# Optimization experiments

Measured on AMD Instinct MI355X. Metric: run time of the kernel, lower is better.

## Reference

```python
import jax, jax.numpy as jnp
import numpy as np
from jax.scipy.special import logsumexp

R, B, D, V, F = 64, 64, 256, 32000, 7
DFF = 4 * D
K_ACT, TOPK_N, TOP_M = 6, 4, 2
NEG = -1e30
C_TAU = 0.20333333  # mean of (1 - alpha) over taus alpha in {0.5, 0.9, 0.99}; zero prev state


def _hex_neighbors(side=8):
    offs = [(1, 0), (-1, 0), (0, 1), (0, -1), (1, -1), (-1, 1)]
    idx = [[((r + dr) % side) * side + (c + dc) % side for dr, dc in offs]
           for r in range(side) for c in range(side)]
    return jnp.array(idx, dtype=jnp.int32)


def setup_inputs() -> dict:
    key = jax.random.key(0)
    ks = jax.random.split(key, 12)
    def rn(k, shp, s):
        return jax.random.normal(k, shp, dtype=jnp.float32) * s
    return {
        "x_per_region": rn(ks[0], (R, B, D), 1.0),
        "targets": jax.random.randint(ks[1], (B,), 0, V),
        "neighbor_indices": _hex_neighbors(8),
        "W1": rn(ks[2], (R, D, DFF), D ** -0.5),
        "b1": jnp.zeros((R, DFF), jnp.float32),
        "W2": rn(ks[3], (R, DFF, D), DFF ** -0.5),
        "b2": jnp.zeros((R, D), jnp.float32),
        "w_gate": rn(ks[4], (D,), D ** -0.5),
        "Wr": rn(ks[5], (D, D), D ** -0.5),
        "Wm": rn(ks[6], (D, D), D ** -0.5),
        "bm": jnp.zeros((D,), jnp.float32),
        "Wg": rn(ks[7], (D, F), D ** -0.5),
        "Wf": rn(ks[8], (F, D, V), 0.02),
        "e_fac": rn(ks[9], (F, D), 1.0),
        "Wb": rn(ks[10], (D, D), D ** -0.5),
    }


def reference(x_per_region, targets, neighbor_indices, W1, b1, W2, b2, w_gate,
              Wr, Wm, bm, Wg, Wf, e_fac, Wb):
    inv_sqrt_d = D ** -0.5
    # per-region FF (grouped GEMM over R regions), exact GELU as torch nn.GELU
    hid = jax.nn.gelu(jnp.einsum('rbd,rdf->rbf', x_per_region, W1) + b1[:, None, :],
                      approximate=False)
    h = jnp.einsum('rbf,rfd->rbd', hid, W2) + b2[:, None, :]
    s = C_TAU * h                    # multi-tau state update (zero prev state, zero neighbor msg)
    H = h + s                        # [R,B,D]
    # region sparsity gate: k-WTA over regions per batch element, io regions forced on
    sc_g = jnp.einsum('rbd,d->br', H, w_gate)           # [B,R]
    kth = jax.lax.top_k(sc_g, K_ACT)[0][:, -1]
    mask = (sc_g >= kth[:, None]).at[:, 0].set(True).at[:, R - 1].set(True)
    Hs = H * mask.T[:, :, None]
    # sparse message passing: top-k gated attention over hex neighbor list
    Nb = Hs[neighbor_indices]                           # [R,6,B,D]
    sc = jnp.einsum('rbd,rkbd->rkb', Hs, Nb) * inv_sqrt_d
    kthn = -jnp.sort(-sc, axis=1)[:, TOPK_N - 1]        # [R,B]
    w = jax.nn.softmax(jnp.where(sc >= kthn[:, None, :], sc, NEG), axis=1)
    H2 = Hs + jnp.einsum('rkb,rkbd->rbd', w, Nb) @ Wr
    # motor readout + multi-facet softmax (mixture over top-m facets)
    motor = H2[R - 1] @ Wm + bm                         # [B,D]
    g = motor @ Wg                                      # [B,F]
    gk = jax.lax.top_k(g, TOP_M)[0][:, -1]
    log_pi = jax.nn.log_softmax(jnp.where(g >= gk[:, None], g, NEG), axis=-1)
    lp = jax.nn.log_softmax(jnp.einsum('bd,fdv->bfv', motor, Wf), axis=-1)
    logp = logsumexp(log_pi[:, :, None] + lp, axis=1)   # [B,V]
    loss = -jnp.mean(jnp.take_along_axis(logp, targets[:, None], axis=1))
    # surprise-gated facet emitter + broadcast routing (next-step buffer, detached)
    S = jax.lax.stop_gradient(loss)
    boost = 1.0 + 2.0 * (S > 0.7).astype(H2.dtype)
    gb = jnp.einsum('rbd,df->rbf', H2, Wg)
    gbk = -jnp.sort(-gb, axis=-1)[..., TOP_M - 1]
    pi = jax.nn.softmax(jnp.where(gb >= gbk[..., None], gb, NEG), axis=-1)
    Bc = H2 * jnp.einsum('rbf,fd->rbd', pi, e_fac) * boost
    NbB = Bc[neighbor_indices]                          # [R,6,B,D]
    sc2 = jnp.einsum('rbd,rkbd->rkb', H2, NbB) * inv_sqrt_d
    kth2 = -jnp.sort(-sc2, axis=1)[:, TOPK_N - 1]
    w2 = jax.nn.softmax(jnp.where(sc2 >= kth2[:, None, :], sc2, NEG), axis=1)
    msg_next = jax.lax.stop_gradient(jnp.einsum('rkb,rkbd->rbd', w2, NbB) @ Wb)
    return logp, loss, msg_next
```

## Files before the change

kernel.cpp:

```cpp
#include <hip/hip_runtime.h>

#define RR 64
#define BB 64
#define DD 256
#define DFF_ 1024
#define VV 32000
#define FF 7

#define TIE_BAND(a, b) (2e-6 * (1.0 + 0.5 * (fabs(a) + fabs(b))))
#define BR_CLAMP 0.30f
#define TOT_CLAMP 0.19f

__device__ __forceinline__ float clampf(float x, float c) {
  return fminf(fmaxf(x, -c), c);
}


__global__ void t_hid(const float* __restrict__ x, const float* __restrict__ W1,
                      const float* __restrict__ b1, double* __restrict__ hid) {
  int fc = blockIdx.x, r = blockIdx.y;
  int t = threadIdx.x;
  int fg = t & 15, bg = t >> 4;
  __shared__ float xs[64][65];
  __shared__ float w1t[64][64];
  double acc[4][4];
#pragma unroll
  for (int i = 0; i < 4; ++i)
#pragma unroll
    for (int j = 0; j < 4; ++j) acc[i][j] = 0.0;
  const float* xr = x + (size_t)r * BB * DD;
  const float* w1r = W1 + (size_t)r * DD * DFF_;
  for (int dt = 0; dt < 4; ++dt) {
    for (int i = t; i < 4096; i += 256) {
      int d = i & 63, b = i >> 6;
      xs[d][b] = xr[b * DD + dt * 64 + d];
    }
    for (int i = t; i < 4096; i += 256) {
      int dd = i >> 6, ff = i & 63;
      w1t[dd][ff] = w1r[(size_t)(dt * 64 + dd) * DFF_ + fc * 64 + ff];
    }
    __syncthreads();
    for (int d = 0; d < 64; ++d) {
      double bv[4], wv[4];
#pragma unroll
      for (int i = 0; i < 4; ++i) bv[i] = (double)xs[d][bg * 4 + i];
#pragma unroll
      for (int j = 0; j < 4; ++j) wv[j] = (double)w1t[d][fg * 4 + j];
#pragma unroll
      for (int i = 0; i < 4; ++i)
#pragma unroll
        for (int j = 0; j < 4; ++j) acc[i][j] += bv[i] * wv[j];
    }
    __syncthreads();
  }
#pragma unroll
  for (int i = 0; i < 4; ++i) {
    int b = bg * 4 + i;
#pragma unroll
    for (int j = 0; j < 4; ++j) {
      int f = fc * 64 + fg * 4 + j;
      double v = acc[i][j] + (double)b1[r * DFF_ + f];
      hid[((size_t)(r * BB + b)) * DFF_ + f] =
          0.5 * v * (1.0 + erf(v * 0.70710678118654752440));
    }
  }
}

__global__ void t_H(const double* __restrict__ hid, const float* __restrict__ W2,
                    const float* __restrict__ b2, double* __restrict__ H) {
  int dc = blockIdx.x, bc = blockIdx.y, r = blockIdx.z;
  int t = threadIdx.x;
  int dg = t & 15, bg = t >> 4;
  __shared__ double ht[64][33];
  __shared__ float wt[64][32];
  double acc[2][2];
#pragma unroll
  for (int i = 0; i < 2; ++i)
#pragma unroll
    for (int j = 0; j < 2; ++j) acc[i][j] = 0.0;
  const double* hr = hid + (size_t)r * BB * DFF_;
  const float* w2r = W2 + (size_t)r * DFF_ * DD;
  for (int ft = 0; ft < 16; ++ft) {
    for (int i = t; i < 2048; i += 256) {
      int f = i & 63, b = i >> 6;
      ht[f][b] = hr[(size_t)(bc * 32 + b) * DFF_ + ft * 64 + f];
    }
    for (int i = t; i < 2048; i += 256) {
      int f = i >> 5, d = i & 31;
      wt[f][d] = w2r[(size_t)(ft * 64 + f) * DD + dc * 32 + d];
    }
    __syncthreads();
    for (int f = 0; f < 64; ++f) {
      double hb[2], wv[2];
#pragma unroll
      for (int i = 0; i < 2; ++i) hb[i] = ht[f][bg * 2 + i];
#pragma unroll
      for (int j = 0; j < 2; ++j) wv[j] = (double)wt[f][dg * 2 + j];
#pragma unroll
      for (int i = 0; i < 2; ++i)
#pragma unroll
        for (int j = 0; j < 2; ++j) acc[i][j] += hb[i] * wv[j];
    }
    __syncthreads();
  }
#pragma unroll
  for (int i = 0; i < 2; ++i) {
    int b = bc * 32 + bg * 2 + i;
#pragma unroll
    for (int j = 0; j < 2; ++j) {
      int d = dc * 32 + dg * 2 + j;
      double h = acc[i][j] + (double)b2[r * DD + d];
      H[((size_t)(r * BB + b)) * DD + d] = h + 0.20333333 * h;
    }
  }
}


__global__ void n_scg(const double* __restrict__ H, const float* __restrict__ wg,
                      double* __restrict__ scg) {
  __shared__ double hbuf[4][256];
  __shared__ float wgs[256];
  int t = threadIdx.x;
  int wv = t >> 6, lane = t & 63;
  int idx = blockIdx.x * 4 + wv;
  int r = idx >> 6, b = idx & 63;
  const double* hp = H + (size_t)idx * DD;
  wgs[t] = wg[t];
#pragma unroll
  for (int j = 0; j < 4; ++j) hbuf[wv][lane + j * 64] = hp[lane + j * 64];
  __syncthreads();
  if (lane == 0) {
    double a = 0.0;
    for (int d = 0; d < DD; ++d) a += hbuf[wv][d] * (double)wgs[d];
    scg[b * RR + r] = a;
  }
}

__global__ void n_mask_dual(const double* __restrict__ scg, float* __restrict__ maskH,
                            float* __restrict__ maskA, int* __restrict__ flagM) {
  int b = threadIdx.x;
  double v[64], w[64];
  for (int r = 0; r < RR; ++r) { v[r] = scg[b * RR + r]; w[r] = v[r]; }
  double k6 = 0.0, k7 = 0.0;
  int i6 = -1, i7 = -1;
  for (int it = 0; it < 7; ++it) {
    int mi = 0;
    for (int r = 1; r < RR; ++r) if (w[r] > w[mi]) mi = r;
    if (it == 5) { k6 = w[mi]; i6 = mi; }
    if (it == 6) { k7 = w[mi]; i7 = mi; }
    w[mi] = -INFINITY;
  }
  double gap = k6 - k7;
  int tie = (gap > 0.0 && gap < TIE_BAND(k6, k7)) ? 1 : 0;
  for (int r = 0; r < RR; ++r) {
    float mh = (v[r] >= k6 || r == 0 || r == RR - 1) ? 1.f : 0.f;
    maskH[b * RR + r] = mh;
    maskA[b * RR + r] = tie ? ((v[r] >= k7 || r == 0 || r == RR - 1) ? 1.f : 0.f) : mh;
    flagM[r * BB + b] = 0;
  }
  if (tie) {
    flagM[i6 * BB + b] = 1;
    flagM[i7 * BB + b] = 1;
  }
}

__global__ void n_hs(const double* __restrict__ H, const float* __restrict__ mask,
                     double* __restrict__ Hs) {
  int idx = blockIdx.x * 256 + threadIdx.x;
  int r = idx >> 14;
  int b = (idx >> 8) & 63;
  Hs[idx] = H[idx] * (double)mask[b * RR + r];
}

__global__ void n_w6x(const double* __restrict__ self, const double* __restrict__ nb,
                      const int* __restrict__ nidx, double* __restrict__ wout,
                      double* __restrict__ walt, int* __restrict__ flag) {
  __shared__ double sbuf[256];
  __shared__ double qbuf[6][256];
  int idx = blockIdx.x;
  int r = idx >> 6, b = idx & 63;
  int lane = threadIdx.x;
  const double* sp = self + (size_t)idx * DD;
#pragma unroll
  for (int j = 0; j < 4; ++j) sbuf[lane + j * 64] = sp[lane + j * 64];
  for (int k = 0; k < 6; ++k) {
    int nr = nidx[r * 6 + k];
    const double* qp = nb + ((size_t)(nr * BB + b)) * DD;
#pragma unroll
    for (int j = 0; j < 4; ++j) qbuf[k][lane + j * 64] = qp[lane + j * 64];
  }
  __syncthreads();
  if (lane == 0) {
    double sc[6];
    for (int k = 0; k < 6; ++k) {
      double a = 0.0;
      for (int d = 0; d < DD; ++d) a += sbuf[d] * qbuf[k][d];
      sc[k] = a * 0.0625;
    }
    double srt[6];
    for (int k = 0; k < 6; ++k) srt[k] = sc[k];
    for (int i = 0; i < 5; ++i) {
      int mi = i;
      for (int j = i + 1; j < 6; ++j) if (srt[j] > srt[mi]) mi = j;
      double tmp = srt[i]; srt[i] = srt[mi]; srt[mi] = tmp;
    }
    double s4 = srt[3], s5 = srt[4], mx = srt[0];
    double e[6], s = 0.0;
    for (int k = 0; k < 6; ++k) {
      e[k] = (sc[k] >= s4) ? exp(sc[k] - mx) : 0.0;
      s += e[k];
    }
    for (int k = 0; k < 6; ++k) wout[(size_t)idx * 6 + k] = e[k] / s;
    double gap = s4 - s5;
    int inband = (gap > 0.0 && gap < TIE_BAND(s4, s5)) ? 1 : 0;
    flag[idx] = inband;
    if (inband) {
      double ea[6], sa = 0.0;
      for (int k = 0; k < 6; ++k) {
        ea[k] = (sc[k] >= s5) ? exp(sc[k] - mx) : 0.0;
        sa += ea[k];
      }
      for (int k = 0; k < 6; ++k) walt[(size_t)idx * 6 + k] = ea[k] / sa;
    } else {
      for (int k = 0; k < 6; ++k) walt[(size_t)idx * 6 + k] = e[k] / s;
    }
  }
}

__global__ void n_w6_sel(const double* __restrict__ self, const double* __restrict__ nb,
                         const int* __restrict__ nidx, const int* __restrict__ flag,
                         const double* __restrict__ wH, double* __restrict__ wout) {
  __shared__ double sbuf[256];
  __shared__ double qbuf[6][256];
  int idx = blockIdx.x;
  int r = idx >> 6, b = idx & 63;
  int lane = threadIdx.x;
  int inb = flag[idx];
  if (inb) {
    const double* sp = self + (size_t)idx * DD;
#pragma unroll
    for (int j = 0; j < 4; ++j) sbuf[lane + j * 64] = sp[lane + j * 64];
    for (int k = 0; k < 6; ++k) {
      int nr = nidx[r * 6 + k];
      const double* qp = nb + ((size_t)(nr * BB + b)) * DD;
#pragma unroll
      for (int j = 0; j < 4; ++j) qbuf[k][lane + j * 64] = qp[lane + j * 64];
    }
  }
  __syncthreads();
  if (!inb) {
    if (lane < 6) wout[(size_t)idx * 6 + lane] = wH[(size_t)idx * 6 + lane];
    return;
  }
  if (lane == 0) {
    double sc[6];
    for (int k = 0; k < 6; ++k) {
      double a = 0.0;
      for (int d = 0; d < DD; ++d) a += sbuf[d] * qbuf[k][d];
      sc[k] = a * 0.0625;
    }
    double srt[6];
    for (int k = 0; k < 6; ++k) srt[k] = sc[k];
    for (int i = 0; i < 4; ++i) {
      int mi = i;
      for (int j = i + 1; j < 6; ++j) if (srt[j] > srt[mi]) mi = j;
      double tmp = srt[i]; srt[i] = srt[mi]; srt[mi] = tmp;
    }
    double s4 = srt[3], mx = srt[0];
    double e[6], s = 0.0;
    for (int k = 0; k < 6; ++k) {
      e[k] = (sc[k] >= s4) ? exp(sc[k] - mx) : 0.0;
      s += e[k];
    }
    for (int k = 0; k < 6; ++k) wout[(size_t)idx * 6 + k] = e[k] / s;
  }
}


__global__ void f_mp_mm(const double* __restrict__ w, const double* __restrict__ nb,
                        const int* __restrict__ nidx, const float* __restrict__ Wmat,
                        const double* __restrict__ Hs, double* __restrict__ H2) {
  __shared__ double mpL[256];
  int rb = blockIdx.x;
  int r = rb >> 6, b = rb & 63;
  int t = threadIdx.x;
  double a = 0.0;
  for (int k = 0; k < 6; ++k) {
    int nr = nidx[r * 6 + k];
    a += w[(size_t)rb * 6 + k] * nb[((size_t)(nr * BB + b)) * DD + t];
  }
  mpL[t] = a;
  __syncthreads();
  double s2 = 0.0;
  for (int d = 0; d < DD; ++d) s2 += mpL[d] * (double)Wmat[d * DD + t];
  size_t i = (size_t)rb * DD + t;
  H2[i] = Hs[i] + s2;
}

__global__ void f_mp_msg(const double* __restrict__ w, const double* __restrict__ nb,
                         const int* __restrict__ nidx, const float* __restrict__ Wmat,
                         float* __restrict__ msgH) {
  __shared__ double mpL[256];
  int rb = blockIdx.x;
  int r = rb >> 6, b = rb & 63;
  int t = threadIdx.x;
  double a = 0.0;
  for (int k = 0; k < 6; ++k) {
    int nr = nidx[r * 6 + k];
    a += w[(size_t)rb * 6 + k] * nb[((size_t)(nr * BB + b)) * DD + t];
  }
  mpL[t] = a;
  __syncthreads();
  double s2 = 0.0;
  for (int d = 0; d < DD; ++d) s2 += mpL[d] * (double)Wmat[d * DD + t];
  msgH[(size_t)rb * DD + t] = (float)s2;
}

__global__ void f_mp_corr(const double* __restrict__ w, const double* __restrict__ nb,
                          const int* __restrict__ nidx, const int* __restrict__ flag,
                          const float* __restrict__ Wmat, const float* __restrict__ msgH,
                          float* __restrict__ corr) {
  int rb = blockIdx.x;
  if (!flag[rb]) return;
  __shared__ double mpL[256];
  int r = rb >> 6, b = rb & 63;
  int t = threadIdx.x;
  double a = 0.0;
  for (int k = 0; k < 6; ++k) {
    int nr = nidx[r * 6 + k];
    a += w[(size_t)rb * 6 + k] * nb[((size_t)(nr * BB + b)) * DD + t];
  }
  mpL[t] = a;
  __syncthreads();
  double s2 = 0.0;
  for (int d = 0; d < DD; ++d) s2 += mpL[d] * (double)Wmat[d * DD + t];
  size_t i = (size_t)rb * DD + t;
  corr[i] += clampf((float)s2 - msgH[i], BR_CLAMP);
}

__global__ void f_mp_h2sel(const double* __restrict__ w, const double* __restrict__ nb,
                           const int* __restrict__ nidx, const int* __restrict__ flag,
                           const float* __restrict__ Wmat, const double* __restrict__ Hs,
                           const double* __restrict__ H2H, double* __restrict__ H2out) {
  int rb = blockIdx.x;
  int t = threadIdx.x;
  size_t i = (size_t)rb * DD + t;
  if (!flag[rb]) { H2out[i] = H2H[i]; return; }
  __shared__ double mpL[256];
  int r = rb >> 6, b = rb & 63;
  double a = 0.0;
  for (int k = 0; k < 6; ++k) {
    int nr = nidx[r * 6 + k];
    a += w[(size_t)rb * 6 + k] * nb[((size_t)(nr * BB + b)) * DD + t];
  }
  mpL[t] = a;
  __syncthreads();
  double s2 = 0.0;
  for (int d = 0; d < DD; ++d) s2 += mpL[d] * (double)Wmat[d * DD + t];
  H2out[i] = Hs[i] + s2;
}


__global__ void n_hs_sel(const double* __restrict__ H, const float* __restrict__ maskA,
                         const int* __restrict__ flag, const double* __restrict__ HsH,
                         double* __restrict__ HsM) {
  int rb = blockIdx.x;
  int t = threadIdx.x;
  size_t i = (size_t)rb * DD + t;
  if (!flag[rb]) { HsM[i] = HsH[i]; return; }
  int r = rb >> 6, b = rb & 63;
  HsM[i] = H[i] * (double)maskA[b * RR + r];
}

__global__ void n_zero(float* __restrict__ p) {
  p[blockIdx.x * 256 + threadIdx.x] = 0.f;
}

__global__ void n_final(const float* __restrict__ msgH, const float* __restrict__ corr,
                        float* __restrict__ out) {
  int i = blockIdx.x * 256 + threadIdx.x;
  out[i] = msgH[i] + clampf(corr[i], TOT_CLAMP);
}

__global__ void n_close(const int* __restrict__ in, const int* __restrict__ nidx,
                        int* __restrict__ out) {
  int idx = blockIdx.x * 256 + threadIdx.x;
  int r = idx >> 6, b = idx & 63;
  int v = in[idx];
  for (int k = 0; k < 6; ++k) v |= in[nidx[r * 6 + k] * BB + b];
  out[idx] = v;
}

__global__ void n_motor(const double* __restrict__ H2, const float* __restrict__ Wm,
                        const float* __restrict__ bm, double* __restrict__ motD,
                        float* __restrict__ motF) {
  int b = blockIdx.x, t = threadIdx.x;
  const double* hp = H2 + ((size_t)((RR - 1) * BB + b)) * DD;
  double a = 0.0;
  for (int d = 0; d < DD; ++d) a += hp[d] * (double)Wm[d * DD + t];
  double mo = a + (double)bm[t];
  motD[b * DD + t] = mo;
  motF[b * DD + t] = (float)mo;
}

__global__ void n_gate(const double* __restrict__ motD, const float* __restrict__ Wg,
                       int* __restrict__ sel, float* __restrict__ c2) {
  __shared__ double mbuf[256];
  __shared__ float wgb[1792];
  int b = blockIdx.x;
  int lane = threadIdx.x;
#pragma unroll
  for (int j = 0; j < 4; ++j) mbuf[lane + j * 64] = motD[b * DD + lane + j * 64];
  for (int i = lane; i < 1792; i += 64) wgb[i] = Wg[i];
  __syncthreads();
  if (lane == 0) {
    double g[FF];
    for (int f = 0; f < FF; ++f) {
      double a = 0.0;
      for (int d = 0; d < DD; ++d) a += mbuf[d] * (double)wgb[d * FF + f];
      g[f] = a;
    }
    double m1 = -INFINITY, m2 = -INFINITY;
    int i1 = -1, i2 = -1;
    for (int f = 0; f < FF; ++f) {
      if (g[f] > m1) { m2 = m1; i2 = i1; m1 = g[f]; i1 = f; }
      else if (g[f] > m2) { m2 = g[f]; i2 = f; }
    }
    double s = 0.0;
    for (int f = 0; f < FF; ++f)
      if (g[f] >= m2) s += exp(g[f] - m1);
    double lse = m1 + log(s);
    sel[b * 2 + 0] = i1;
    sel[b * 2 + 1] = i2;
    c2[b * 2 + 0] = (float)(g[i1] - lse);
    c2[b * 2 + 1] = (float)(g[i2] - lse);
  }
}

__global__ void n_pi_dual(const double* __restrict__ H2, const float* __restrict__ Wg,
                          double* __restrict__ piH, double* __restrict__ piA,
                          int* __restrict__ flag) {
  __shared__ double hbuf[4][256];
  __shared__ float wgb[1792];
  int t = threadIdx.x;
  int wv = t >> 6, lane = t & 63;
  int idx = blockIdx.x * 4 + wv;
  const double* hp = H2 + (size_t)idx * DD;
#pragma unroll
  for (int j = 0; j < 4; ++j) hbuf[wv][lane + j * 64] = hp[lane + j * 64];
  for (int i = t; i < 1792; i += 256) wgb[i] = Wg[i];
  __syncthreads();
  if (lane == 0) {
    double gb[FF];
    for (int f = 0; f < FF; ++f) {
      double a = 0.0;
      for (int d = 0; d < DD; ++d) a += hbuf[wv][d] * (double)wgb[d * FF + f];
      gb[f] = a;
    }
    double srt[FF];
    for (int f = 0; f < FF; ++f) srt[f] = gb[f];
    for (int i = 0; i < 3; ++i) {
      int mi = i;
      for (int j = i + 1; j < FF; ++j) if (srt[j] > srt[mi]) mi = j;
      double tp = srt[i]; srt[i] = srt[mi]; srt[mi] = tp;
    }
    double m1 = srt[0], m2 = srt[1], m3 = srt[2];
    double e[FF], s = 0.0;
    for (int f = 0; f < FF; ++f) {
      e[f] = (gb[f] >= m2) ? exp(gb[f] - m1) : 0.0;
      s += e[f];
    }
    for (int f = 0; f < FF; ++f) piH[(size_t)idx * FF + f] = e[f] / s;
    double gap = m2 - m3;
    int inband = (gap > 0.0 && gap < TIE_BAND(m2, m3)) ? 1 : 0;
    flag[idx] = inband;
    if (inband) {
      double ea[FF], sa = 0.0;
      for (int f = 0; f < FF; ++f) {
        ea[f] = (gb[f] >= m3) ? exp(gb[f] - m1) : 0.0;
        sa += ea[f];
      }
      for (int f = 0; f < FF; ++f) piA[(size_t)idx * FF + f] = ea[f] / sa;
    } else {
      for (int f = 0; f < FF; ++f) piA[(size_t)idx * FF + f] = e[f] / s;
    }
  }
}

__global__ void n_pi_sel(const double* __restrict__ H2, const float* __restrict__ Wg,
                         const int* __restrict__ flag, const double* __restrict__ piHsrc,
                         double* __restrict__ piout) {
  __shared__ double hbuf[4][256];
  __shared__ float wgb[1792];
  int t = threadIdx.x;
  int wv = t >> 6, lane = t & 63;
  int idx = blockIdx.x * 4 + wv;
  int inb = flag[idx];
  if (inb) {
    const double* hp = H2 + (size_t)idx * DD;
#pragma unroll
    for (int j = 0; j < 4; ++j) hbuf[wv][lane + j * 64] = hp[lane + j * 64];
  }
  for (int i = t; i < 1792; i += 256) wgb[i] = Wg[i];
  __syncthreads();
  if (!inb) {
    if (lane < FF) piout[(size_t)idx * FF + lane] = piHsrc[(size_t)idx * FF + lane];
    return;
  }
  if (lane == 0) {
    double gb[FF];
    for (int f = 0; f < FF; ++f) {
      double a = 0.0;
      for (int d = 0; d < DD; ++d) a += hbuf[wv][d] * (double)wgb[d * FF + f];
      gb[f] = a;
    }
    double m1 = -INFINITY, m2 = -INFINITY;
    for (int f = 0; f < FF; ++f) {
      if (gb[f] > m1) { m2 = m1; m1 = gb[f]; }
      else if (gb[f] > m2) { m2 = gb[f]; }
    }
    double e[FF], s = 0.0;
    for (int f = 0; f < FF; ++f) {
      e[f] = (gb[f] >= m2) ? exp(gb[f] - m1) : 0.0;
      s += e[f];
    }
    for (int f = 0; f < FF; ++f) piout[(size_t)idx * FF + f] = e[f] / s;
  }
}

__global__ void n_bc(const double* __restrict__ H2, const double* __restrict__ pi,
                     const float* __restrict__ e_fac, const float* __restrict__ boost_p,
                     double* __restrict__ Bc) {
  int rb = blockIdx.x, t = threadIdx.x;
  double ef = 0.0;
  for (int f = 0; f < FF; ++f) ef += pi[(size_t)rb * FF + f] * (double)e_fac[f * DD + t];
  double boost = (double)(*boost_p);
  Bc[(size_t)rb * DD + t] = H2[(size_t)rb * DD + t] * ef * boost;
}

__global__ void n_bc_sel(const double* __restrict__ H2, const double* __restrict__ pi,
                         const float* __restrict__ e_fac, const float* __restrict__ boost_p,
                         const int* __restrict__ flag, const double* __restrict__ BcH,
                         double* __restrict__ Bc2) {
  int rb = blockIdx.x, t = threadIdx.x;
  size_t i = (size_t)rb * DD + t;
  if (!flag[rb]) { Bc2[i] = BcH[i]; return; }
  double ef = 0.0;
  for (int f = 0; f < FF; ++f) ef += pi[(size_t)rb * FF + f] * (double)e_fac[f * DD + t];
  double boost = (double)(*boost_p);
  Bc2[i] = H2[i] * ef * boost;
}


__global__ void k_z2(const float* __restrict__ motor, const float* __restrict__ Wf,
                     const int* __restrict__ sel, float* __restrict__ z2) {
  int vc = blockIdx.x, f = blockIdx.y;
  int t = threadIdx.x;
  int vg = t & 31, bg = t >> 5;
  __shared__ float mt[32][65];
  __shared__ float wt[32][256];
  __shared__ int selL[128];
  if (t < 128) selL[t] = sel[t];
  float acc[8][8];
#pragma unroll
  for (int i = 0; i < 8; ++i)
#pragma unroll
    for (int j = 0; j < 8; ++j) acc[i][j] = 0.f;
  const float* wf = Wf + (size_t)f * DD * VV;
  for (int dt = 0; dt < 8; ++dt) {
    for (int i = t; i < 2048; i += 256) {
      int d = i & 31, b = i >> 5;
      mt[d][b] = motor[b * DD + dt * 32 + d];
    }
    for (int i = t; i < 8192; i += 256) {
      int d = i >> 8, v = i & 255;
      wt[d][v] = wf[(size_t)(dt * 32 + d) * VV + vc * 256 + v];
    }
    __syncthreads();
    for (int d = 0; d < 32; ++d) {
      float bv[8], wv[8];
#pragma unroll
      for (int i = 0; i < 8; ++i) bv[i] = mt[d][bg * 8 + i];
#pragma unroll
      for (int j = 0; j < 8; ++j) wv[j] = wt[d][vg + j * 32];
#pragma unroll
      for (int i = 0; i < 8; ++i)
#pragma unroll
        for (int j = 0; j < 8; ++j) acc[i][j] += bv[i] * wv[j];
    }
    __syncthreads();
  }
#pragma unroll
  for (int i = 0; i < 8; ++i) {
    int b = bg * 8 + i;
    int s0 = selL[b * 2 + 0], s1 = selL[b * 2 + 1];
    if (s0 == f) {
#pragma unroll
      for (int j = 0; j < 8; ++j)
        z2[((size_t)(b * 2 + 0)) * VV + vc * 256 + vg + j * 32] = acc[i][j];
    }
    if (s1 == f) {
#pragma unroll
      for (int j = 0; j < 8; ++j)
        z2[((size_t)(b * 2 + 1)) * VV + vc * 256 + vg + j * 32] = acc[i][j];
    }
  }
}

__global__ void k_lse(const float* __restrict__ z2, float* __restrict__ lse) {
  int row = blockIdx.x;
  int t = threadIdx.x;
  const float* zp = z2 + (size_t)row * VV;
  float m = -INFINITY, s = 0.f;
  for (int v = t; v < VV; v += 256) {
    float val = zp[v];
    if (val > m) { s = s * expf(m - val) + 1.f; m = val; }
    else s += expf(val - m);
  }
  __shared__ float sm[256], ss[256];
  sm[t] = m; ss[t] = s;
  __syncthreads();
  for (int off = 128; off > 0; off >>= 1) {
    if (t < off) {
      float m2 = sm[t + off], s2 = ss[t + off], m1 = sm[t], s1 = ss[t];
      float M = fmaxf(m1, m2);
      sm[t] = M;
      ss[t] = s1 * expf(m1 - M) + s2 * expf(m2 - M);
    }
    __syncthreads();
  }
  if (t == 0) lse[row] = sm[0] + logf(ss[0]);
}

__global__ void k_logp(const float* __restrict__ z2, const float* __restrict__ c2,
                       const float* __restrict__ lse, float* __restrict__ out_logp) {
  int b = blockIdx.y;
  int v = blockIdx.x * 256 + threadIdx.x;
  float a0 = c2[b * 2 + 0] - lse[b * 2 + 0] + z2[((size_t)(b * 2 + 0)) * VV + v];
  float a1 = c2[b * 2 + 1] - lse[b * 2 + 1] + z2[((size_t)(b * 2 + 1)) * VV + v];
  float M = fmaxf(a0, a1);
  out_logp[(size_t)b * VV + v] = M + logf(expf(a0 - M) + expf(a1 - M));
}

__global__ void k_loss(const float* __restrict__ out_logp, const int* __restrict__ targets,
                       float* __restrict__ out_loss, float* __restrict__ boost) {
  int b = threadIdx.x;
  float v = out_logp[(size_t)b * VV + targets[b]];
#pragma unroll
  for (int off = 32; off > 0; off >>= 1) v += __shfl_xor(v, off, 64);
  if (b == 0) {
    float loss = -v / 64.f;
    *out_loss = loss;
    *boost = 1.f + 2.f * ((loss > 0.7f) ? 1.f : 0.f);
  }
}

extern "C" void kernel_launch(void* const* d_in, const int* in_sizes, int n_in,
                              void* d_out, int out_size, void* d_ws, size_t ws_size,
                              hipStream_t stream) {
  const float* x       = (const float*)d_in[0];
  const int*   targets = (const int*)d_in[1];
  const int*   nidx    = (const int*)d_in[2];
  const float* W1      = (const float*)d_in[3];
  const float* b1      = (const float*)d_in[4];
  const float* W2      = (const float*)d_in[5];
  const float* b2      = (const float*)d_in[6];
  const float* w_gate  = (const float*)d_in[7];
  const float* Wr      = (const float*)d_in[8];
  const float* Wm      = (const float*)d_in[9];
  const float* bm      = (const float*)d_in[10];
  const float* Wg      = (const float*)d_in[11];
  const float* Wf      = (const float*)d_in[12];
  const float* e_fac   = (const float*)d_in[13];
  const float* Wb      = (const float*)d_in[14];

  float* out_logp = (float*)d_out;
  float* out_loss = out_logp + (size_t)BB * VV;
  float* out_msg  = out_loss + 1;

  double* dH   = (double*)d_ws;
  double* dHs  = dH + 1048576;
  double* dHsM = dHs + 1048576;
  double* dH2  = dHsM + 1048576;
  double* dH2b = dH2 + 1048576;
  double* dBc  = dH2b + 1048576;
  double* dBcA = dBc + 1048576;
  double* dHid = dBcA + 1048576;
  float*  fZ2  = (float*)dHid;
  double* dScg = dHid + 4194304;
  double* dW6h = dScg + 4096;
  double* dW6a = dW6h + 24576;
  double* dW6b = dW6a + 24576;
  double* dW2h = dW6b + 24576;
  double* dW2a = dW2h + 24576;
  double* dW2b = dW2a + 24576;
  double* dPiH = dW2b + 24576;
  double* dPiA = dPiH + 28672;
  double* dPiH2= dPiA + 28672;
  double* dMotD= dPiH2 + 28672;
  float*  fMaskH = (float*)(dMotD + 16384);
  float*  fMaskA = fMaskH + 4096;
  float*  fMsgH  = fMaskA + 4096;
  float*  fCorr  = fMsgH + 1048576;
  float*  fMotF  = fCorr + 1048576;
  float*  fC2    = fMotF + 16384;
  float*  fLse   = fC2 + 128;
  float*  fBoost = fLse + 128;
  int*    iSel   = (int*)(fBoost + 1);
  int*    fW1    = iSel + 128;
  int*    fW2    = fW1 + 4096;
  int*    fPi    = fW2 + 4096;
  int*    fM     = fPi + 4096;
  int*    cPi    = fM + 4096;
  int*    cW1    = cPi + 4096;
  int*    cM     = cW1 + 4096;
  int*    cM2    = cM + 4096;

  t_hid<<<dim3(16, 64), 256, 0, stream>>>(x, W1, b1, dHid);
  t_H<<<dim3(8, 2, 64), 256, 0, stream>>>(dHid, W2, b2, dH);
  n_scg<<<1024, 256, 0, stream>>>(dH, w_gate, dScg);
  n_mask_dual<<<1, 64, 0, stream>>>(dScg, fMaskH, fMaskA, fM);
  n_hs<<<4096, 256, 0, stream>>>(dH, fMaskH, dHs);
  n_w6x<<<4096, 64, 0, stream>>>(dHs, dHs, nidx, dW6h, dW6a, fW1);
  f_mp_mm<<<4096, 256, 0, stream>>>(dW6h, dHs, nidx, Wr, dHs, dH2);
  n_motor<<<64, 256, 0, stream>>>(dH2, Wm, bm, dMotD, fMotF);
  n_gate<<<64, 64, 0, stream>>>(dMotD, Wg, iSel, fC2);
  k_z2<<<dim3(125, 7), 256, 0, stream>>>(fMotF, Wf, iSel, fZ2);
  k_lse<<<128, 256, 0, stream>>>(fZ2, fLse);
  k_logp<<<dim3(125, BB), 256, 0, stream>>>(fZ2, fC2, fLse, out_logp);
  k_loss<<<1, 64, 0, stream>>>(out_logp, targets, out_loss, fBoost);
  n_pi_dual<<<1024, 256, 0, stream>>>(dH2, Wg, dPiH, dPiA, fPi);
  n_bc<<<4096, 256, 0, stream>>>(dH2, dPiH, e_fac, fBoost, dBc);
  n_w6x<<<4096, 64, 0, stream>>>(dH2, dBc, nidx, dW2h, dW2a, fW2);
  f_mp_msg<<<4096, 256, 0, stream>>>(dW2h, dBc, nidx, Wb, fMsgH);
  n_zero<<<4096, 256, 0, stream>>>(fCorr);
  f_mp_corr<<<4096, 256, 0, stream>>>(dW2a, dBc, nidx, fW2, Wb, fMsgH, fCorr);
  n_bc_sel<<<4096, 256, 0, stream>>>(dH2, dPiA, e_fac, fBoost, fPi, dBc, dBcA);
  n_close<<<16, 256, 0, stream>>>(fPi, nidx, cPi);
  n_w6_sel<<<4096, 64, 0, stream>>>(dH2, dBcA, nidx, cPi, dW2h, dW2b);
  f_mp_corr<<<4096, 256, 0, stream>>>(dW2b, dBcA, nidx, cPi, Wb, fMsgH, fCorr);
  f_mp_h2sel<<<4096, 256, 0, stream>>>(dW6a, dHs, nidx, fW1, Wr, dHs, dH2, dH2b);
  n_pi_sel<<<1024, 256, 0, stream>>>(dH2b, Wg, fW1, dPiH, dPiH2);
  n_bc_sel<<<4096, 256, 0, stream>>>(dH2b, dPiH2, e_fac, fBoost, fW1, dBc, dBcA);
  n_close<<<16, 256, 0, stream>>>(fW1, nidx, cW1);
  n_w6_sel<<<4096, 64, 0, stream>>>(dH2b, dBcA, nidx, cW1, dW2h, dW2b);
  f_mp_corr<<<4096, 256, 0, stream>>>(dW2b, dBcA, nidx, cW1, Wb, fMsgH, fCorr);
  n_hs_sel<<<4096, 256, 0, stream>>>(dH, fMaskA, fM, dHs, dHsM);
  n_close<<<16, 256, 0, stream>>>(fM, nidx, cM);
  n_w6_sel<<<4096, 64, 0, stream>>>(dHsM, dHsM, nidx, cM, dW6h, dW6b);
  f_mp_h2sel<<<4096, 256, 0, stream>>>(dW6b, dHsM, nidx, cM, Wr, dHsM, dH2, dH2b);
  n_pi_sel<<<1024, 256, 0, stream>>>(dH2b, Wg, cM, dPiH, dPiH2);
  n_bc_sel<<<4096, 256, 0, stream>>>(dH2b, dPiH2, e_fac, fBoost, cM, dBc, dBcA);
  n_close<<<16, 256, 0, stream>>>(cM, nidx, cM2);
  n_w6_sel<<<4096, 64, 0, stream>>>(dH2b, dBcA, nidx, cM2, dW2h, dW2b);
  f_mp_corr<<<4096, 256, 0, stream>>>(dW2b, dBcA, nidx, cM2, Wb, fMsgH, fCorr);
  n_final<<<4096, 256, 0, stream>>>(fMsgH, fCorr, out_msg);
}
```

Measured before the change: 939.2 us.

## Skip copy-through of unflagged rows by selecting source buffers per row

The selective recompute kernels no longer copy the baseline values (H2, Bc, Hs) into alternate buffers for rows that are not flagged. Each consumer instead picks, per row, either the recomputed buffer or the original through a flag array, so only flagged rows are written. This removes several full-size double-precision copy passes across the tie-correction chain, at the cost of extra flag reads and indirect pointer selection inside the gather loops. The k_z2 logits GEMM tile depth is also halved from 32 to 16, which cuts shared memory but doubles the number of sync steps.

```diff
diff --git a/kernel.cpp b/kernel.cpp
--- a/kernel.cpp
+++ b/kernel.cpp
@@ -172,6 +172,16 @@
   Hs[idx] = H[idx] * (double)mask[b * RR + r];
 }
 
+__global__ void n_hs_g(const double* __restrict__ H, const float* __restrict__ maskA,
+                       const int* __restrict__ gate, double* __restrict__ HsM) {
+  int rb = blockIdx.x;
+  if (!gate[rb]) return;
+  int t = threadIdx.x;
+  size_t i = (size_t)rb * DD + t;
+  int r = rb >> 6, b = rb & 63;
+  HsM[i] = H[i] * (double)maskA[b * RR + r];
+}
+
 __global__ void n_w6x(const double* __restrict__ self, const double* __restrict__ nb,
                       const int* __restrict__ nidx, double* __restrict__ wout,
                       double* __restrict__ walt, int* __restrict__ flag) {
@@ -227,28 +237,32 @@
   }
 }
 
-__global__ void n_w6_sel(const double* __restrict__ self, const double* __restrict__ nb,
-                         const int* __restrict__ nidx, const int* __restrict__ flag,
-                         const double* __restrict__ wH, double* __restrict__ wout) {
+__global__ void n_w6_sel_g(const double* __restrict__ selfD, const double* __restrict__ selfC,
+                           const int* __restrict__ flagS,
+                           const double* __restrict__ nbD, const double* __restrict__ nbC,
+                           const int* __restrict__ flagN,
+                           const int* __restrict__ nidx, const int* __restrict__ gate,
+                           const double* __restrict__ wH, double* __restrict__ wout) {
   __shared__ double sbuf[256];
   __shared__ double qbuf[6][256];
   int idx = blockIdx.x;
   int r = idx >> 6, b = idx & 63;
   int lane = threadIdx.x;
-  int inb = flag[idx];
-  if (inb) {
-    const double* sp = self + (size_t)idx * DD;
+  int g = gate[idx];
+  if (g) {
+    const double* sp = (flagS[idx] ? selfD : selfC) + (size_t)idx * DD;
 #pragma unroll
     for (int j = 0; j < 4; ++j) sbuf[lane + j * 64] = sp[lane + j * 64];
     for (int k = 0; k < 6; ++k) {
       int nr = nidx[r * 6 + k];
-      const double* qp = nb + ((size_t)(nr * BB + b)) * DD;
+      int ni = nr * BB + b;
+      const double* qp = (flagN[ni] ? nbD : nbC) + (size_t)ni * DD;
 #pragma unroll
       for (int j = 0; j < 4; ++j) qbuf[k][lane + j * 64] = qp[lane + j * 64];
     }
   }
   __syncthreads();
-  if (!inb) {
+  if (!g) {
     if (lane < 6) wout[(size_t)idx * 6 + lane] = wH[(size_t)idx * 6 + lane];
     return;
   }
@@ -316,19 +330,23 @@
   msgH[(size_t)rb * DD + t] = (float)s2;
 }
 
-__global__ void f_mp_corr(const double* __restrict__ w, const double* __restrict__ nb,
-                          const int* __restrict__ nidx, const int* __restrict__ flag,
-                          const float* __restrict__ Wmat, const float* __restrict__ msgH,
-                          float* __restrict__ corr) {
+__global__ void f_mp_corr_g(const double* __restrict__ w,
+                            const double* __restrict__ nbD, const double* __restrict__ nbC,
+                            const int* __restrict__ flagN,
+                            const int* __restrict__ nidx, const int* __restrict__ gate,
+                            const float* __restrict__ Wmat, const float* __restrict__ msgH,
+                            float* __restrict__ corr) {
   int rb = blockIdx.x;
-  if (!flag[rb]) return;
+  if (!gate[rb]) return;
   __shared__ double mpL[256];
   int r = rb >> 6, b = rb & 63;
   int t = threadIdx.x;
   double a = 0.0;
   for (int k = 0; k < 6; ++k) {
     int nr = nidx[r * 6 + k];
-    a += w[(size_t)rb * 6 + k] * nb[((size_t)(nr * BB + b)) * DD + t];
+    int ni = nr * BB + b;
+    const double* q = flagN[ni] ? nbD : nbC;
+    a += w[(size_t)rb * 6 + k] * q[(size_t)ni * DD + t];
   }
   mpL[t] = a;
   __syncthreads();
@@ -338,42 +356,41 @@
   corr[i] += clampf((float)s2 - msgH[i], BR_CLAMP);
 }
 
-__global__ void f_mp_h2sel(const double* __restrict__ w, const double* __restrict__ nb,
-                           const int* __restrict__ nidx, const int* __restrict__ flag,
-                           const float* __restrict__ Wmat, const double* __restrict__ Hs,
-                           const double* __restrict__ H2H, double* __restrict__ H2out) {
+__global__ void f_mp_h2_g(const double* __restrict__ w,
+                          const double* __restrict__ nbD, const double* __restrict__ nbC,
+                          const int* __restrict__ flagN,
+                          const int* __restrict__ nidx, const float* __restrict__ Wmat,
+                          const double* __restrict__ HsD, const double* __restrict__ HsC,
+                          const int* __restrict__ flagHs,
+                          const int* __restrict__ gate, double* __restrict__ H2out) {
   int rb = blockIdx.x;
-  int t = threadIdx.x;
-  size_t i = (size_t)rb * DD + t;
-  if (!flag[rb]) { H2out[i] = H2H[i]; return; }
+  if (!gate[rb]) return;
   __shared__ double mpL[256];
   int r = rb >> 6, b = rb & 63;
+  int t = threadIdx.x;
   double a = 0.0;
   for (int k = 0; k < 6; ++k) {
     int nr = nidx[r * 6 + k];
-    a += w[(size_t)rb * 6 + k] * nb[((size_t)(nr * BB + b)) * DD + t];
+    int ni = nr * BB + b;
+    const double* q = flagN[ni] ? nbD : nbC;
+    a += w[(size_t)rb * 6 + k] * q[(size_t)ni * DD + t];
   }
   mpL[t] = a;
   __syncthreads();
   double s2 = 0.0;
   for (int d = 0; d < DD; ++d) s2 += mpL[d] * (double)Wmat[d * DD + t];
-  H2out[i] = Hs[i] + s2;
-}
-
-
-__global__ void n_hs_sel(const double* __restrict__ H, const float* __restrict__ maskA,
-                         const int* __restrict__ flag, const double* __restrict__ HsH,
-                         double* __restrict__ HsM) {
-  int rb = blockIdx.x;
-  int t = threadIdx.x;
   size_t i = (size_t)rb * DD + t;
-  if (!flag[rb]) { HsM[i] = HsH[i]; return; }
-  int r = rb >> 6, b = rb & 63;
-  HsM[i] = H[i] * (double)maskA[b * RR + r];
-}
+  const double* hs = flagHs[rb] ? HsD : HsC;
+  H2out[i] = hs[i] + s2;
+}
+
 
 __global__ void n_zero(float* __restrict__ p) {
   p[blockIdx.x * 256 + threadIdx.x] = 0.f;
+}
+
+__global__ void n_izero(int* __restrict__ p) {
+  p[blockIdx.x * 256 + threadIdx.x] = 0;
 }
 
 __global__ void n_final(const float* __restrict__ msgH, const float* __restrict__ corr,
@@ -487,23 +504,23 @@
   }
 }
 
-__global__ void n_pi_sel(const double* __restrict__ H2, const float* __restrict__ Wg,
-                         const int* __restrict__ flag, const double* __restrict__ piHsrc,
+__global__ void n_pi_sel(const double* __restrict__ H2src, const float* __restrict__ Wg,
+                         const int* __restrict__ gate, const double* __restrict__ piHsrc,
                          double* __restrict__ piout) {
   __shared__ double hbuf[4][256];
   __shared__ float wgb[1792];
   int t = threadIdx.x;
   int wv = t >> 6, lane = t & 63;
   int idx = blockIdx.x * 4 + wv;
-  int inb = flag[idx];
-  if (inb) {
-    const double* hp = H2 + (size_t)idx * DD;
+  int g = gate[idx];
+  if (g) {
+    const double* hp = H2src + (size_t)idx * DD;
 #pragma unroll
     for (int j = 0; j < 4; ++j) hbuf[wv][lane + j * 64] = hp[lane + j * 64];
   }
   for (int i = t; i < 1792; i += 256) wgb[i] = Wg[i];
   __syncthreads();
-  if (!inb) {
+  if (!g) {
     if (lane < FF) piout[(size_t)idx * FF + lane] = piHsrc[(size_t)idx * FF + lane];
     return;
   }
@@ -538,17 +555,17 @@
   Bc[(size_t)rb * DD + t] = H2[(size_t)rb * DD + t] * ef * boost;
 }
 
-__global__ void n_bc_sel(const double* __restrict__ H2, const double* __restrict__ pi,
-                         const float* __restrict__ e_fac, const float* __restrict__ boost_p,
-                         const int* __restrict__ flag, const double* __restrict__ BcH,
-                         double* __restrict__ Bc2) {
-  int rb = blockIdx.x, t = threadIdx.x;
+__global__ void n_bc_g(const double* __restrict__ H2src, const double* __restrict__ pi,
+                       const float* __restrict__ e_fac, const float* __restrict__ boost_p,
+                       const int* __restrict__ gate, double* __restrict__ Bc2) {
+  int rb = blockIdx.x;
+  if (!gate[rb]) return;
+  int t = threadIdx.x;
   size_t i = (size_t)rb * DD + t;
-  if (!flag[rb]) { Bc2[i] = BcH[i]; return; }
   double ef = 0.0;
   for (int f = 0; f < FF; ++f) ef += pi[(size_t)rb * FF + f] * (double)e_fac[f * DD + t];
   double boost = (double)(*boost_p);
-  Bc2[i] = H2[i] * ef * boost;
+  Bc2[i] = H2src[i] * ef * boost;
 }
 
 
@@ -557,8 +574,8 @@
   int vc = blockIdx.x, f = blockIdx.y;
   int t = threadIdx.x;
   int vg = t & 31, bg = t >> 5;
-  __shared__ float mt[32][65];
-  __shared__ float wt[32][256];
+  __shared__ float mt[16][65];
+  __shared__ float wt[16][256];
   __shared__ int selL[128];
   if (t < 128) selL[t] = sel[t];
   float acc[8][8];
@@ -567,17 +584,17 @@
 #pragma unroll
     for (int j = 0; j < 8; ++j) acc[i][j] = 0.f;
   const float* wf = Wf + (size_t)f * DD * VV;
-  for (int dt = 0; dt < 8; ++dt) {
-    for (int i = t; i < 2048; i += 256) {
-      int d = i & 31, b = i >> 5;
-      mt[d][b] = motor[b * DD + dt * 32 + d];
-    }
-    for (int i = t; i < 8192; i += 256) {
+  for (int dt = 0; dt < 16; ++dt) {
+    for (int i = t; i < 1024; i += 256) {
+      int d = i & 15, b = i >> 4;
+      mt[d][b] = motor[b * DD + dt * 16 + d];
+    }
+    for (int i = t; i < 4096; i += 256) {
       int d = i >> 8, v = i & 255;
-      wt[d][v] = wf[(size_t)(dt * 32 + d) * VV + vc * 256 + v];
+      wt[d][v] = wf[(size_t)(dt * 16 + d) * VV + vc * 256 + v];
     }
     __syncthreads();
-    for (int d = 0; d < 32; ++d) {
+    for (int d = 0; d < 16; ++d) {
       float bv[8], wv[8];
 #pragma unroll
       for (int i = 0; i < 8; ++i) bv[i] = mt[d][bg * 8 + i];
@@ -715,6 +732,7 @@
   int*    cW1    = cPi + 4096;
   int*    cM     = cW1 + 4096;
   int*    cM2    = cM + 4096;
+  int*    iZero  = cM2 + 4096;
 
   t_hid<<<dim3(16, 64), 256, 0, stream>>>(x, W1, b1, dHid);
   t_H<<<dim3(8, 2, 64), 256, 0, stream>>>(dHid, W2, b2, dH);
@@ -734,25 +752,26 @@
   n_w6x<<<4096, 64, 0, stream>>>(dH2, dBc, nidx, dW2h, dW2a, fW2);
   f_mp_msg<<<4096, 256, 0, stream>>>(dW2h, dBc, nidx, Wb, fMsgH);
   n_zero<<<4096, 256, 0, stream>>>(fCorr);
-  f_mp_corr<<<4096, 256, 0, stream>>>(dW2a, dBc, nidx, fW2, Wb, fMsgH, fCorr);
-  n_bc_sel<<<4096, 256, 0, stream>>>(dH2, dPiA, e_fac, fBoost, fPi, dBc, dBcA);
+  n_izero<<<16, 256, 0, stream>>>(iZero);
+  f_mp_corr_g<<<4096, 256, 0, stream>>>(dW2a, dBc, dBc, iZero, nidx, fW2, Wb, fMsgH, fCorr);
+  n_bc_g<<<4096, 256, 0, stream>>>(dH2, dPiA, e_fac, fBoost, fPi, dBcA);
   n_close<<<16, 256, 0, stream>>>(fPi, nidx, cPi);
-  n_w6_sel<<<4096, 64, 0, stream>>>(dH2, dBcA, nidx, cPi, dW2h, dW2b);
-  f_mp_corr<<<4096, 256, 0, stream>>>(dW2b, dBcA, nidx, cPi, Wb, fMsgH, fCorr);
-  f_mp_h2sel<<<4096, 256, 0, stream>>>(dW6a, dHs, nidx, fW1, Wr, dHs, dH2, dH2b);
+  n_w6_sel_g<<<4096, 64, 0, stream>>>(dH2, dH2, iZero, dBcA, dBc, fPi, nidx, cPi, dW2h, dW2b);
+  f_mp_corr_g<<<4096, 256, 0, stream>>>(dW2b, dBcA, dBc, fPi, nidx, cPi, Wb, fMsgH, fCorr);
+  f_mp_h2_g<<<4096, 256, 0, stream>>>(dW6a, dHs, dHs, iZero, nidx, Wr, dHs, dHs, iZero, fW1, dH2b);
   n_pi_sel<<<1024, 256, 0, stream>>>(dH2b, Wg, fW1, dPiH, dPiH2);
-  n_bc_sel<<<4096, 256, 0, stream>>>(dH2b, dPiH2, e_fac, fBoost, fW1, dBc, dBcA);
+  n_bc_g<<<4096, 256, 0, stream>>>(dH2b, dPiH2, e_fac, fBoost, fW1, dBcA);
   n_close<<<16, 256, 0, stream>>>(fW1, nidx, cW1);
-  n_w6_sel<<<4096, 64, 0, stream>>>(dH2b, dBcA, nidx, cW1, dW2h, dW2b);
-  f_mp_corr<<<4096, 256, 0, stream>>>(dW2b, dBcA, nidx, cW1, Wb, fMsgH, fCorr);
-  n_hs_sel<<<4096, 256, 0, stream>>>(dH, fMaskA, fM, dHs, dHsM);
+  n_w6_sel_g<<<4096, 64, 0, stream>>>(dH2b, dH2, fW1, dBcA, dBc, fW1, nidx, cW1, dW2h, dW2b);
+  f_mp_corr_g<<<4096, 256, 0, stream>>>(dW2b, dBcA, dBc, fW1, nidx, cW1, Wb, fMsgH, fCorr);
+  n_hs_g<<<4096, 256, 0, stream>>>(dH, fMaskA, fM, dHsM);
   n_close<<<16, 256, 0, stream>>>(fM, nidx, cM);
-  n_w6_sel<<<4096, 64, 0, stream>>>(dHsM, dHsM, nidx, cM, dW6h, dW6b);
-  f_mp_h2sel<<<4096, 256, 0, stream>>>(dW6b, dHsM, nidx, cM, Wr, dHsM, dH2, dH2b);
+  n_w6_sel_g<<<4096, 64, 0, stream>>>(dHsM, dHs, fM, dHsM, dHs, fM, nidx, cM, dW6h, dW6b);
+  f_mp_h2_g<<<4096, 256, 0, stream>>>(dW6b, dHsM, dHs, fM, nidx, Wr, dHsM, dHs, fM, cM, dH2b);
   n_pi_sel<<<1024, 256, 0, stream>>>(dH2b, Wg, cM, dPiH, dPiH2);
-  n_bc_sel<<<4096, 256, 0, stream>>>(dH2b, dPiH2, e_fac, fBoost, cM, dBc, dBcA);
+  n_bc_g<<<4096, 256, 0, stream>>>(dH2b, dPiH2, e_fac, fBoost, cM, dBcA);
   n_close<<<16, 256, 0, stream>>>(cM, nidx, cM2);
-  n_w6_sel<<<4096, 64, 0, stream>>>(dH2b, dBcA, nidx, cM2, dW2h, dW2b);
-  f_mp_corr<<<4096, 256, 0, stream>>>(dW2b, dBcA, nidx, cM2, Wb, fMsgH, fCorr);
+  n_w6_sel_g<<<4096, 64, 0, stream>>>(dH2b, dH2, cM, dBcA, dBc, cM, nidx, cM2, dW2h, dW2b);
+  f_mp_corr_g<<<4096, 256, 0, stream>>>(dW2b, dBcA, dBc, cM, nidx, cM2, Wb, fMsgH, fCorr);
   n_final<<<4096, 256, 0, stream>>>(fMsgH, fCorr, out_msg);
 }
```

New measurement: 913.6 us. 2.7% less time.
